# Kernel optimization log

Hardware: AMD Instinct MI355X
Metric: run time of the kernel (lower is better)

The kernel has to match this reference:

```python
import jax, jax.numpy as jnp
import numpy as np
from jax import lax

# init_kwargs constants
DO_TUBE = False
TAU = 0.3
ITERATIONS = 5
BLEND_FACTOR = 0.3


def _avg_pool3(x):
    """3x3x3 avg pool, stride 1, zero padding 1, count_include_pad=True.
    x: (n, h, w, d). Matches torch F.avg_pool3d(kernel=3, stride=1, padding=1)."""
    s = lax.reduce_window(x, 0.0, lax.add, (1, 3, 3, 3), (1, 1, 1, 1), 'SAME')
    return s * (1.0 / 27.0)


def setup_inputs() -> dict:
    key = jax.random.key(0)
    # binary mask (b, 1, h, w, d) as docstring requires
    u = jax.random.uniform(key, (2, 1, 256, 256, 256), dtype=jnp.float32)
    seg = (u > 0.5).astype(jnp.float32)
    return {"segmentation": seg}


def reference(segmentation):
    b, c, h, w, d = segmentation.shape
    x = segmentation.reshape(b * c, h, w, d)

    # NOTE: in the original code `mask` is never updated inside the iteration
    # loop, so every iteration adds the identical term; the loop over the
    # batch dim is also trivially batchable. Compute the per-iteration term
    # once (fully batched) and scale by ITERATIONS.
    eroded = -_avg_pool3(-x)            # differentiable erosion
    dilated = _avg_pool3(eroded)        # differentiable dilation
    diff = x - dilated
    term = jax.nn.sigmoid((diff - 0.5) / TAU) + diff  # soft_threshold + residual
    skeleton = ITERATIONS * term

    skeleton = skeleton.reshape(b, c, h, w, d)
    # DO_TUBE is False (the torch code path for True is broken for 5D input)
    skeleton = BLEND_FACTOR * segmentation + (1.0 - BLEND_FACTOR) * skeleton
    skeleton = jnp.round(jnp.clip(skeleton, 0.0, 1.0))
    return 1.0 - skeleton
```

## Files before the change

kernel.cpp:

```cpp
#include <hip/hip_runtime.h>
#include <stdint.h>


typedef float        vfloat4 __attribute__((ext_vector_type(4)));
typedef unsigned int vuint4  __attribute__((ext_vector_type(4)));

#define CH2 32
#define BLOCKS 1024

__global__ __launch_bounds__(256) void skel_fused(const float* __restrict__ x,
                                                  float* __restrict__ outp) {
    const int ln  = threadIdx.x & 63;
    const int wv  = threadIdx.x >> 6;
    const int bid = blockIdx.x;
    const int L      = (bid & 7) * 128 + (bid >> 3);
    const int wblock = L >> 4;
    const int combo  = L & 15;
    const int b      = combo & 1;
    const int hc     = combo >> 1;
    const int w      = wblock * 4 + wv;
    const int h0     = hc * CH2;
    const int hlast  = (h0 + CH2 + 1 > 255) ? 255 : (h0 + CH2 + 1);

    const vfloat4* __restrict__ xs = (const vfloat4*)x;
    vfloat4* __restrict__ os = (vfloat4*)outp;
    const uint32_t rbase = (uint32_t)b * 4194304u + (uint32_t)w * 64u + (uint32_t)ln;
    const vfloat4 vzero = {0.0f, 0.0f, 0.0f, 0.0f};

    int  co[5]; bool cv[5];
    #pragma unroll
    for (int j = 0; j < 5; ++j) {
        int wj = w + j - 2;
        cv[j]  = (wj >= 0) && (wj <= 255);
        int wc = wj < 0 ? 0 : (wj > 255 ? 255 : wj);
        co[j]  = (wc - w) * 64;
    }

    auto load5 = [&](int hp, vfloat4 R[5]) {
        int hcl = hp < 0 ? 0 : (hp > hlast ? hlast : hp);
        uint32_t rb = rbase + (uint32_t)hcl * 16384u;
        #pragma unroll
        for (int j = 0; j < 5; ++j) {
            vfloat4 v = xs[(int)rb + co[j]];
            R[j] = cv[j] ? v : vzero;
        }
    };

    auto dw_from = [&](const vfloat4 R[5], int hp) -> uint32_t {
        if (hp < 0 || hp > 255) return 0u;
        vfloat4 s = R[0] + R[4] + 2.0f * (R[1] + R[3]) + 3.0f * R[2];
        if (w == 0 || w == 255) s = s - R[2];
        uint32_t tn = (uint32_t)s.x | ((uint32_t)s.y << 8)
                    | ((uint32_t)s.z << 16) | ((uint32_t)s.w << 24);
        vuint4 u2 = __builtin_bit_cast(vuint4, R[2]);
        uint32_t tx = ((u2.x >> 22) & 0x80u)    | ((u2.y >> 14) & 0x8000u)
                    | ((u2.z >> 6) & 0x800000u) | ((u2.w << 2) & 0x80000000u);
        uint32_t up = (uint32_t)__shfl_up((int)tn, 1);
        uint32_t dn = (uint32_t)__shfl_down((int)tn, 1);
        if (ln == 0)  up = 0u;
        if (ln == 63) dn = 0u;
        uint64_t W = (uint64_t)(up >> 16) | ((uint64_t)tn << 16)
                   | ((uint64_t)(dn & 0xffffu) << 48);
        uint64_t S = W + ((W >> 8) << 1) + (W >> 16) * 3u + ((W >> 24) << 1) + (W >> 32);
        uint32_t n = (uint32_t)S;
        if (ln == 0)  n -= (tn & 0xffu);
        if (ln == 63) n -= (tn & 0xff000000u);
        return n | tx;
    };

    auto emit = [&](int h, uint32_t a0, uint32_t a1, uint32_t a2,
                    uint32_t a3, uint32_t a4) {
        uint32_t m0 = a0 & 0x7f7f7f7fu, m1 = a1 & 0x7f7f7f7fu, m2 = a2 & 0x7f7f7f7fu,
                 m3 = a3 & 0x7f7f7f7fu, m4 = a4 & 0x7f7f7f7fu;
        uint32_t e0 = m0 & 0x00ff00ffu, e1 = m1 & 0x00ff00ffu, e2 = m2 & 0x00ff00ffu,
                 e3 = m3 & 0x00ff00ffu, e4 = m4 & 0x00ff00ffu;
        uint32_t o0 = (m0 >> 8) & 0x00ff00ffu, o1 = (m1 >> 8) & 0x00ff00ffu,
                 o2 = (m2 >> 8) & 0x00ff00ffu, o3 = (m3 >> 8) & 0x00ff00ffu,
                 o4 = (m4 >> 8) & 0x00ff00ffu;
        uint32_t ae = e0 + e4 + ((e1 + e3) << 1) + e2 * 3u;
        uint32_t ao = o0 + o4 + ((o1 + o3) << 1) + o2 * 3u;
        if (h == 0 || h == 255) { ae -= e2; ao -= o2; }
        vfloat4 o;
        o.x = (((ae & 0xffffu) >= 9u) && !(a2 & 0x80u))       ? 1.0f : 0.0f;
        o.y = (((ao & 0xffffu) >= 9u) && !(a2 & 0x8000u))     ? 1.0f : 0.0f;
        o.z = (((ae >> 16) >= 9u)     && !(a2 & 0x800000u))   ? 1.0f : 0.0f;
        o.w = (((ao >> 16) >= 9u)     && !(a2 & 0x80000000u)) ? 1.0f : 0.0f;
        __builtin_nontemporal_store(o, &os[rbase + (uint32_t)h * 16384u]);
    };

    vfloat4 B0[5], B1[5], B2[5], B3[5];
    uint32_t d0, d1, d2, d3, d4, d5, d6, d7;
    load5(h0 - 2, B0); load5(h0 - 1, B1); load5(h0, B2); load5(h0 + 1, B3);
    d0 = dw_from(B0, h0 - 2); load5(h0 + 2, B0);
    d1 = dw_from(B1, h0 - 1); load5(h0 + 3, B1);
    d2 = dw_from(B2, h0    ); load5(h0 + 4, B2);
    d3 = dw_from(B3, h0 + 1); load5(h0 + 5, B3);

    for (int h = h0; h < h0 + CH2; h += 4) {
        d4 = dw_from(B0, h + 2); load5(h + 6, B0); emit(h,     d0, d1, d2, d3, d4);
        d5 = dw_from(B1, h + 3); load5(h + 7, B1); emit(h + 1, d1, d2, d3, d4, d5);
        d6 = dw_from(B2, h + 4); load5(h + 8, B2); emit(h + 2, d2, d3, d4, d5, d6);
        d7 = dw_from(B3, h + 5); load5(h + 9, B3); emit(h + 3, d3, d4, d5, d6, d7);
        d0 = d4; d1 = d5; d2 = d6; d3 = d7;
    }
}

extern "C" void kernel_launch(void* const* d_in, const int* in_sizes, int n_in,
                              void* d_out, int out_size, void* d_ws, size_t ws_size,
                              hipStream_t stream) {
    const float* x = (const float*)d_in[0];
    skel_fused<<<BLOCKS, 256, 0, stream>>>(x, (float*)d_out);
}
```

Measured before the change: 279.6 us.

## Stage input rows in LDS via global_load_lds with double buffering

Replaces each wave's five redundant neighbour-column global loads with a shared LDS tile. The tile is filled by direct global-to-LDS loads, and each of the four waves stages two of the eight needed columns. The row loop becomes a double-buffered pipeline with a block barrier per row, and the dilation/erosion sums read neighbours from LDS. This cuts redundant global/L2 reads, but adds a barrier per row and shrinks the prefetch depth from four rows ahead to one.

```diff
diff --git a/kernel.cpp b/kernel.cpp
--- a/kernel.cpp
+++ b/kernel.cpp
@@ -10,6 +10,7 @@
 
 __global__ __launch_bounds__(256) void skel_fused(const float* __restrict__ x,
                                                   float* __restrict__ outp) {
+    __shared__ vfloat4 lds[2][8][64];
     const int ln  = threadIdx.x & 63;
     const int wv  = threadIdx.x >> 6;
     const int bid = blockIdx.x;
@@ -18,36 +19,49 @@
     const int combo  = L & 15;
     const int b      = combo & 1;
     const int hc     = combo >> 1;
-    const int w      = wblock * 4 + wv;
+    const int w0b    = wblock * 4;
+    const int w      = w0b + wv;
     const int h0     = hc * CH2;
-    const int hlast  = (h0 + CH2 + 1 > 255) ? 255 : (h0 + CH2 + 1);
 
     const vfloat4* __restrict__ xs = (const vfloat4*)x;
     vfloat4* __restrict__ os = (vfloat4*)outp;
     const uint32_t rbase = (uint32_t)b * 4194304u + (uint32_t)w * 64u + (uint32_t)ln;
     const vfloat4 vzero = {0.0f, 0.0f, 0.0f, 0.0f};
 
-    int  co[5]; bool cv[5];
+    const int sr0 = w0b - 2 + 2 * wv, sr1 = sr0 + 1;
+    const int sc0 = sr0 < 0 ? 0 : (sr0 > 255 ? 255 : sr0);
+    const int sc1 = sr1 < 0 ? 0 : (sr1 > 255 ? 255 : sr1);
+    const uint32_t sb0 = (uint32_t)b * 4194304u + (uint32_t)sc0 * 64u + (uint32_t)ln;
+    const uint32_t sb1 = (uint32_t)b * 4194304u + (uint32_t)sc1 * 64u + (uint32_t)ln;
+
+    auto stage = [&](int hp, int buf) {
+        int hcl = hp < 0 ? 0 : (hp > 255 ? 255 : hp);
+        uint32_t off = (uint32_t)hcl * 16384u;
+        __builtin_amdgcn_global_load_lds(
+            (const __attribute__((address_space(1))) void*)&xs[sb0 + off],
+            (__attribute__((address_space(3))) void*)&lds[buf][2 * wv][0],
+            16, 0, 0);
+        __builtin_amdgcn_global_load_lds(
+            (const __attribute__((address_space(1))) void*)&xs[sb1 + off],
+            (__attribute__((address_space(3))) void*)&lds[buf][2 * wv + 1][0],
+            16, 0, 0);
+    };
+
+    bool cv[5];
     #pragma unroll
     for (int j = 0; j < 5; ++j) {
         int wj = w + j - 2;
-        cv[j]  = (wj >= 0) && (wj <= 255);
-        int wc = wj < 0 ? 0 : (wj > 255 ? 255 : wj);
-        co[j]  = (wc - w) * 64;
+        cv[j] = (wj >= 0) && (wj <= 255);
     }
 
-    auto load5 = [&](int hp, vfloat4 R[5]) {
-        int hcl = hp < 0 ? 0 : (hp > hlast ? hlast : hp);
-        uint32_t rb = rbase + (uint32_t)hcl * 16384u;
+    auto dw_from = [&](int buf, int hp) -> uint32_t {
+        if (hp < 0 || hp > 255) return 0u;
+        vfloat4 R[5];
         #pragma unroll
         for (int j = 0; j < 5; ++j) {
-            vfloat4 v = xs[(int)rb + co[j]];
+            vfloat4 v = lds[buf][wv + j][ln];
             R[j] = cv[j] ? v : vzero;
         }
-    };
-
-    auto dw_from = [&](const vfloat4 R[5], int hp) -> uint32_t {
-        if (hp < 0 || hp > 255) return 0u;
         vfloat4 s = R[0] + R[4] + 2.0f * (R[1] + R[3]) + 3.0f * R[2];
         if (w == 0 || w == 255) s = s - R[2];
         uint32_t tn = (uint32_t)s.x | ((uint32_t)s.y << 8)
@@ -88,20 +102,19 @@
         __builtin_nontemporal_store(o, &os[rbase + (uint32_t)h * 16384u]);
     };
 
-    vfloat4 B0[5], B1[5], B2[5], B3[5];
-    uint32_t d0, d1, d2, d3, d4, d5, d6, d7;
-    load5(h0 - 2, B0); load5(h0 - 1, B1); load5(h0, B2); load5(h0 + 1, B3);
-    d0 = dw_from(B0, h0 - 2); load5(h0 + 2, B0);
-    d1 = dw_from(B1, h0 - 1); load5(h0 + 3, B1);
-    d2 = dw_from(B2, h0    ); load5(h0 + 4, B2);
-    d3 = dw_from(B3, h0 + 1); load5(h0 + 5, B3);
-
-    for (int h = h0; h < h0 + CH2; h += 4) {
-        d4 = dw_from(B0, h + 2); load5(h + 6, B0); emit(h,     d0, d1, d2, d3, d4);
-        d5 = dw_from(B1, h + 3); load5(h + 7, B1); emit(h + 1, d1, d2, d3, d4, d5);
-        d6 = dw_from(B2, h + 4); load5(h + 8, B2); emit(h + 2, d2, d3, d4, d5, d6);
-        d7 = dw_from(B3, h + 5); load5(h + 9, B3); emit(h + 3, d3, d4, d5, d6, d7);
-        d0 = d4; d1 = d5; d2 = d6; d3 = d7;
+    stage(h0 - 2, 0);
+    __syncthreads();
+    stage(h0 - 1, 1);
+    uint32_t d0 = 0, d1 = 0, d2 = 0, d3 = 0;
+    int cur = 0;
+    const int plast = h0 + CH2 + 1;
+    for (int p = h0 - 2; p <= plast; ++p) {
+        uint32_t d4 = dw_from(cur, p);
+        if (p >= h0 + 2) emit(p - 2, d0, d1, d2, d3, d4);
+        __syncthreads();
+        if (p + 2 <= plast) stage(p + 2, cur);
+        cur ^= 1;
+        d0 = d1; d1 = d2; d2 = d3; d3 = d4;
     }
 }
 
```

Result: faster. 240.0 us (-14.1%).
